# Optimization experiments

Hardware: AMD Instinct MI355X
Metric: run time of the kernel (lower is better)

The kernel has to match this reference:

```python
import jax, jax.numpy as jnp
import numpy as np

MODEL_DIM = 1024
DK = 1024
DV = 1024
B, S = 4, 2048

def setup_inputs() -> dict:
    key = jax.random.key(0)
    ks = jax.random.split(key, 9)
    return {
        "q": jax.random.normal(ks[0], (B, S, MODEL_DIM), dtype=jnp.float32),
        "k": jax.random.normal(ks[1], (B, S, MODEL_DIM), dtype=jnp.float32),
        "v": jax.random.normal(ks[2], (B, S, MODEL_DIM), dtype=jnp.float32),
        "Wq": jax.random.normal(ks[3], (MODEL_DIM, DK), dtype=jnp.float32),
        "Wk": jax.random.normal(ks[4], (MODEL_DIM, DK), dtype=jnp.float32),
        "Wv": jax.random.normal(ks[5], (MODEL_DIM, DV), dtype=jnp.float32),
        "bq": jax.random.normal(ks[6], (DK,), dtype=jnp.float32),
        "bk": jax.random.normal(ks[7], (DK,), dtype=jnp.float32),
        "bv": jax.random.normal(ks[8], (DV,), dtype=jnp.float32),
    }

def reference(q, k, v, Wq, Wk, Wv, bq, bk, bv):
    # Linear projections
    Q = q @ Wq + bq  # [B,S,dk]
    K = k @ Wk + bk  # [B,S,dk]
    V = v @ Wv + bv  # [B,S,dv]
    # NOTE: original scales by 1/sqrt(model_dim), not 1/sqrt(dk)
    scale = 1.0 / jnp.sqrt(jnp.float32(MODEL_DIM))
    score = jnp.einsum("bqd,bkd->bqk", Q, K) * scale  # [B,S,S]
    attn = jax.nn.softmax(score, axis=-1)
    return jnp.einsum("bqk,bkd->bqd", attn, V)  # [B,S,dv]
```

## Files before the change

kernel.cpp:

```cpp
#include <hip/hip_runtime.h>
#include <stdint.h>


typedef __attribute__((ext_vector_type(8))) short short8;
typedef __attribute__((ext_vector_type(4))) float f32x4;
typedef __attribute__((ext_vector_type(4))) unsigned short us4;

#define BM 128
#define BN 128
#define BK 32

static __device__ __forceinline__ unsigned short f2bf(float f) {
  unsigned x = __builtin_bit_cast(unsigned, f);
  x += 0x7fffu + ((x >> 16) & 1u);
  return (unsigned short)(x >> 16);
}
static __device__ __forceinline__ float bf2f(unsigned short u) {
  return __builtin_bit_cast(float, (unsigned)u << 16);
}

static __device__ __forceinline__ void gload_lds16(void* lds, const void* g) {
  __builtin_amdgcn_global_load_lds(
      (const __attribute__((address_space(1))) unsigned int*)g,
      (__attribute__((address_space(3))) unsigned int*)lds, 16, 0, 0);
}

__global__ void __launch_bounds__(256)
split_hl(const float* __restrict__ x, unsigned short* __restrict__ h,
         unsigned short* __restrict__ l, int n4) {
  int i = blockIdx.x * 256 + threadIdx.x;
  if (i >= n4) return;
  float4 v = ((const float4*)x)[i];
  float vv[4] = {v.x, v.y, v.z, v.w};
  us4 hh, ll;
#pragma unroll
  for (int j = 0; j < 4; ++j) {
    unsigned short hi = f2bf(vv[j]);
    hh[j] = hi;
    ll[j] = f2bf(vv[j] - bf2f(hi));
  }
  *(us4*)(h + (size_t)i * 4) = hh;
  *(us4*)(l + (size_t)i * 4) = ll;
}

__global__ void __launch_bounds__(256)
wsplit_t(const float* __restrict__ W, unsigned short* __restrict__ th,
         unsigned short* __restrict__ tl, int K, int N) {
  __shared__ float tile[64][65];
  int k0 = blockIdx.y * 64, n0 = blockIdx.x * 64;
  int t = threadIdx.x;
#pragma unroll
  for (int i = 0; i < 16; ++i) {
    int idx = t + i * 256;
    int r = idx >> 6, c = idx & 63;
    tile[r][c] = W[(size_t)(k0 + r) * N + n0 + c];
  }
  __syncthreads();
#pragma unroll
  for (int i = 0; i < 16; ++i) {
    int idx = t + i * 256;
    int nn = idx >> 6, kk = idx & 63;
    float v = tile[kk][nn];
    unsigned short hi = f2bf(v);
    size_t o = (size_t)(n0 + nn) * K + k0 + kk;
    th[o] = hi;
    tl[o] = f2bf(v - bf2f(hi));
  }
}

template <int MODE>
__global__ void __launch_bounds__(256)
gemm_split(const unsigned short* __restrict__ Ah, const unsigned short* __restrict__ Al,
           const unsigned short* __restrict__ Bh, const unsigned short* __restrict__ Bl,
           long sAb, long sBb, int M, int N, int K,
           const float* __restrict__ bias, float scale,
           float* __restrict__ outF, long sOb,
           unsigned short* __restrict__ outH, unsigned short* __restrict__ outL,
           int Srows) {
  __shared__ __align__(16) unsigned short At[BM * BK];
  __shared__ __align__(16) unsigned short Bt[BN * BK];
  const int t = threadIdx.x;
  const int wave = t >> 6, lane = t & 63;
  const int wr = (wave >> 1) * 64, wc = (wave & 1) * 64;
  const long zb = blockIdx.z;
  const int m0 = blockIdx.y * BM, n0 = blockIdx.x * BN;
  Ah += zb * sAb; Al += zb * sAb;
  Bh += zb * sBb; Bl += zb * sBb;

  f32x4 acc[4][4] = {};

  const unsigned short* Ap[3] = {Ah, Ah, Al};
  const unsigned short* Bp[3] = {Bh, Bl, Bh};

  const int lrow = lane & 15, lk = lane >> 4;
  const int c0 = wave * 64 + lane;
  char* AtB = (char*)At;
  char* BtB = (char*)Bt;

  for (int p = 0; p < 3; ++p) {
    const unsigned short* Ac = Ap[p];
    const unsigned short* Bc = Bp[p];
    for (int kt = 0; kt < K; kt += BK) {
#pragma unroll
      for (int i = 0; i < 2; ++i) {
        int c = i * 256 + c0;
        gload_lds16(AtB + (size_t)(i * 256 + wave * 64) * 16,
                    Ac + (size_t)(m0 + (c >> 2)) * K + kt + (c & 3) * 8);
        gload_lds16(BtB + (size_t)(i * 256 + wave * 64) * 16,
                    Bc + (size_t)(n0 + (c >> 2)) * K + kt + (c & 3) * 8);
      }
      __syncthreads();
      short8 af[4], bfr[4];
#pragma unroll
      for (int m = 0; m < 4; ++m)
        af[m] = *(const short8*)(AtB + (size_t)((wr + m * 16 + lrow) * 64 + lk * 16));
#pragma unroll
      for (int n = 0; n < 4; ++n)
        bfr[n] = *(const short8*)(BtB + (size_t)((wc + n * 16 + lrow) * 64 + lk * 16));
#pragma unroll
      for (int m = 0; m < 4; ++m)
#pragma unroll
        for (int n = 0; n < 4; ++n)
          acc[m][n] = __builtin_amdgcn_mfma_f32_16x16x32_bf16(af[m], bfr[n], acc[m][n], 0, 0, 0);
      __syncthreads();
    }
  }

#pragma unroll
  for (int m = 0; m < 4; ++m) {
#pragma unroll
    for (int n = 0; n < 4; ++n) {
      int gcol = n0 + wc + n * 16 + lrow;
      float bv = bias ? bias[gcol] : 0.0f;
#pragma unroll
      for (int r = 0; r < 4; ++r) {
        int grow = m0 + wr + m * 16 + lk * 4 + r;
        float v = acc[m][n][r] * scale + bv;
        if (MODE == 0) {
          outF[zb * sOb + (size_t)grow * N + gcol] = v;
        } else if (MODE == 1) {
          unsigned short hi = f2bf(v);
          size_t o = (size_t)grow * N + gcol;
          outH[o] = hi;
          outL[o] = f2bf(v - bf2f(hi));
        } else {
          int bb = grow / Srows, s = grow - bb * Srows;
          size_t o = (size_t)bb * N * Srows + (size_t)gcol * Srows + s;
          unsigned short hi = f2bf(v);
          outH[o] = hi;
          outL[o] = f2bf(v - bf2f(hi));
        }
      }
    }
  }
}

__global__ void __launch_bounds__(256)
softmax_rows(const float* __restrict__ sc, unsigned short* __restrict__ ph,
             unsigned short* __restrict__ pl, int S) {
  const size_t row = blockIdx.x;
  const float* sr = sc + row * S;
  int t = threadIdx.x;
  float x[8];
  const float4* s4 = (const float4*)sr;
#pragma unroll
  for (int i = 0; i < 2; ++i) {
    float4 v = s4[t + i * 256];
    x[i * 4 + 0] = v.x; x[i * 4 + 1] = v.y; x[i * 4 + 2] = v.z; x[i * 4 + 3] = v.w;
  }
  float m = x[0];
#pragma unroll
  for (int j = 1; j < 8; ++j) m = fmaxf(m, x[j]);
#pragma unroll
  for (int off = 32; off; off >>= 1) m = fmaxf(m, __shfl_xor(m, off));
  __shared__ float red[4];
  if ((t & 63) == 0) red[t >> 6] = m;
  __syncthreads();
  m = fmaxf(fmaxf(red[0], red[1]), fmaxf(red[2], red[3]));
  float e[8];
  float sum = 0.f;
#pragma unroll
  for (int j = 0; j < 8; ++j) { e[j] = __expf(x[j] - m); sum += e[j]; }
#pragma unroll
  for (int off = 32; off; off >>= 1) sum += __shfl_xor(sum, off);
  __shared__ float red2[4];
  if ((t & 63) == 0) red2[t >> 6] = sum;
  __syncthreads();
  sum = red2[0] + red2[1] + red2[2] + red2[3];
  float rinv = 1.0f / sum;
#pragma unroll
  for (int i = 0; i < 2; ++i) {
    us4 hh, ll;
#pragma unroll
    for (int j = 0; j < 4; ++j) {
      float p = e[i * 4 + j] * rinv;
      unsigned short hi = f2bf(p);
      hh[j] = hi;
      ll[j] = f2bf(p - bf2f(hi));
    }
    size_t o = row * S + (size_t)(t + i * 256) * 4;
    *(us4*)(ph + o) = hh;
    *(us4*)(pl + o) = ll;
  }
}

extern "C" void kernel_launch(void* const* d_in, const int* in_sizes, int n_in,
                              void* d_out, int out_size, void* d_ws, size_t ws_size,
                              hipStream_t stream) {
  const int B = 4, S = 2048, D = 1024, DK = 1024, DV = 1024;
  const float* q = (const float*)d_in[0];
  const float* k = (const float*)d_in[1];
  const float* v = (const float*)d_in[2];
  const float* Wq = (const float*)d_in[3];
  const float* Wk = (const float*)d_in[4];
  const float* Wv = (const float*)d_in[5];
  const float* bq = (const float*)d_in[6];
  const float* bk = (const float*)d_in[7];
  const float* bv = (const float*)d_in[8];

  char* ws = (char*)d_ws;
  const size_t MBy = 1024 * 1024;
  unsigned short* qh = (unsigned short*)(ws + 0 * MBy);
  unsigned short* ql = (unsigned short*)(ws + 16 * MBy);
  unsigned short* kh = (unsigned short*)(ws + 32 * MBy);
  unsigned short* kl = (unsigned short*)(ws + 48 * MBy);
  unsigned short* vh = (unsigned short*)(ws + 64 * MBy);
  unsigned short* vl = (unsigned short*)(ws + 80 * MBy);
  unsigned short* wqth = (unsigned short*)(ws + 96 * MBy);
  unsigned short* wqtl = (unsigned short*)(ws + 98 * MBy);
  unsigned short* wkth = (unsigned short*)(ws + 100 * MBy);
  unsigned short* wktl = (unsigned short*)(ws + 102 * MBy);
  unsigned short* wvth = (unsigned short*)(ws + 104 * MBy);
  unsigned short* wvtl = (unsigned short*)(ws + 106 * MBy);
  unsigned short* Qh = (unsigned short*)(ws + 108 * MBy);
  unsigned short* Ql = (unsigned short*)(ws + 124 * MBy);
  unsigned short* Kh = (unsigned short*)(ws + 140 * MBy);
  unsigned short* Kl = (unsigned short*)(ws + 156 * MBy);
  unsigned short* Vth = (unsigned short*)(ws + 172 * MBy);
  unsigned short* Vtl = (unsigned short*)(ws + 188 * MBy);
  float* scores = (float*)(ws + 0 * MBy);
  unsigned short* Ph = (unsigned short*)(ws + 64 * MBy);
  unsigned short* Pl = (unsigned short*)(ws + 108 * MBy);

  const int n4 = B * S * D / 4;
  split_hl<<<n4 / 256, 256, 0, stream>>>(q, qh, ql, n4);
  split_hl<<<n4 / 256, 256, 0, stream>>>(k, kh, kl, n4);
  split_hl<<<n4 / 256, 256, 0, stream>>>(v, vh, vl, n4);

  wsplit_t<<<dim3(DK / 64, D / 64), 256, 0, stream>>>(Wq, wqth, wqtl, D, DK);
  wsplit_t<<<dim3(DK / 64, D / 64), 256, 0, stream>>>(Wk, wkth, wktl, D, DK);
  wsplit_t<<<dim3(DV / 64, D / 64), 256, 0, stream>>>(Wv, wvth, wvtl, D, DV);

  gemm_split<1><<<dim3(DK / BN, (B * S) / BM, 1), 256, 0, stream>>>(
      qh, ql, wqth, wqtl, 0, 0, B * S, DK, D, bq, 1.0f, nullptr, 0, Qh, Ql, S);
  gemm_split<1><<<dim3(DK / BN, (B * S) / BM, 1), 256, 0, stream>>>(
      kh, kl, wkth, wktl, 0, 0, B * S, DK, D, bk, 1.0f, nullptr, 0, Kh, Kl, S);
  gemm_split<2><<<dim3(DV / BN, (B * S) / BM, 1), 256, 0, stream>>>(
      vh, vl, wvth, wvtl, 0, 0, B * S, DV, D, bv, 1.0f, nullptr, 0, Vth, Vtl, S);

  gemm_split<0><<<dim3(S / BN, S / BM, B), 256, 0, stream>>>(
      Qh, Ql, Kh, Kl, (long)S * DK, (long)S * DK, S, S, DK, nullptr, 0.03125f,
      scores, (long)S * S, nullptr, nullptr, S);

  softmax_rows<<<B * S, 256, 0, stream>>>(scores, Ph, Pl, S);

  gemm_split<0><<<dim3(DV / BN, S / BM, B), 256, 0, stream>>>(
      Ph, Pl, Vth, Vtl, (long)S * S, (long)DV * S, S, DV, S, nullptr, 1.0f,
      (float*)d_out, (long)S * DV, nullptr, nullptr, S);
}
```

Before: 774.4 us.

## Fuse split-bf16 passes into one K loop and swizzle LDS tiles

Instead of three separate K sweeps (hi*hi, hi*lo, lo*hi), each K step now loads all four hi/lo tiles into a 32KB shared buffer and runs the three MFMA products from LDS. This cuts barrier count and loop overhead threefold, and each tile is fetched once per K step instead of being refetched across passes. An XOR swizzle on the 16-byte chunk slot is applied to both the global-to-LDS loads and the fragment reads to reduce LDS bank conflicts. LDS usage doubles, which may reduce occupancy.

```diff
diff --git a/kernel.cpp b/kernel.cpp
--- a/kernel.cpp
+++ b/kernel.cpp
@@ -77,8 +77,7 @@
            float* __restrict__ outF, long sOb,
            unsigned short* __restrict__ outH, unsigned short* __restrict__ outL,
            int Srows) {
-  __shared__ __align__(16) unsigned short At[BM * BK];
-  __shared__ __align__(16) unsigned short Bt[BN * BK];
+  __shared__ __align__(16) unsigned short Lds[4 * BM * BK];
   const int t = threadIdx.x;
   const int wave = t >> 6, lane = t & 63;
   const int wr = (wave >> 1) * 64, wc = (wave & 1) * 64;
@@ -89,41 +88,49 @@
 
   f32x4 acc[4][4] = {};
 
-  const unsigned short* Ap[3] = {Ah, Ah, Al};
-  const unsigned short* Bp[3] = {Bh, Bl, Bh};
-
   const int lrow = lane & 15, lk = lane >> 4;
-  const int c0 = wave * 64 + lane;
-  char* AtB = (char*)At;
-  char* BtB = (char*)Bt;
-
-  for (int p = 0; p < 3; ++p) {
-    const unsigned short* Ac = Ap[p];
-    const unsigned short* Bc = Bp[p];
-    for (int kt = 0; kt < K; kt += BK) {
-#pragma unroll
-      for (int i = 0; i < 2; ++i) {
-        int c = i * 256 + c0;
-        gload_lds16(AtB + (size_t)(i * 256 + wave * 64) * 16,
-                    Ac + (size_t)(m0 + (c >> 2)) * K + kt + (c & 3) * 8);
-        gload_lds16(BtB + (size_t)(i * 256 + wave * 64) * 16,
-                    Bc + (size_t)(n0 + (c >> 2)) * K + kt + (c & 3) * 8);
-      }
-      __syncthreads();
+  char* AhT = (char*)Lds;
+  char* AlT = AhT + 8192;
+  char* BhT = AlT + 8192;
+  char* BlT = BhT + 8192;
+
+  const int sw = (lrow >> 1) & 3;
+  const int slotB16 = (lk ^ sw) * 16;
+
+  for (int kt = 0; kt < K; kt += BK) {
+#pragma unroll
+    for (int i = 0; i < 2; ++i) {
+      int c = i * 256 + t;
+      int row = c >> 2;
+      int cs = (c & 3) ^ ((c >> 3) & 3);
+      size_t ldsOff = (size_t)(i * 256 + wave * 64) * 16;
+      size_t gA = (size_t)(m0 + row) * K + kt + cs * 8;
+      size_t gB = (size_t)(n0 + row) * K + kt + cs * 8;
+      gload_lds16(AhT + ldsOff, Ah + gA);
+      gload_lds16(AlT + ldsOff, Al + gA);
+      gload_lds16(BhT + ldsOff, Bh + gB);
+      gload_lds16(BlT + ldsOff, Bl + gB);
+    }
+    __syncthreads();
+
+    const char* Ap[3] = {AhT, AhT, AlT};
+    const char* Bp[3] = {BhT, BlT, BhT};
+#pragma unroll
+    for (int p = 0; p < 3; ++p) {
       short8 af[4], bfr[4];
 #pragma unroll
       for (int m = 0; m < 4; ++m)
-        af[m] = *(const short8*)(AtB + (size_t)((wr + m * 16 + lrow) * 64 + lk * 16));
+        af[m] = *(const short8*)(Ap[p] + (size_t)((wr + m * 16 + lrow) * 64) + slotB16);
 #pragma unroll
       for (int n = 0; n < 4; ++n)
-        bfr[n] = *(const short8*)(BtB + (size_t)((wc + n * 16 + lrow) * 64 + lk * 16));
+        bfr[n] = *(const short8*)(Bp[p] + (size_t)((wc + n * 16 + lrow) * 64) + slotB16);
 #pragma unroll
       for (int m = 0; m < 4; ++m)
 #pragma unroll
         for (int n = 0; n < 4; ++n)
           acc[m][n] = __builtin_amdgcn_mfma_f32_16x16x32_bf16(af[m], bfr[n], acc[m][n], 0, 0, 0);
-      __syncthreads();
-    }
+    }
+    __syncthreads();
   }
 
 #pragma unroll
```

Measured after the change: 620.1 us. 19.9% less time.
